# Kernel tuning notes

Hardware: AMD Instinct MI355X
Metric: run time of the kernel (lower is better)

## Reference

```python
import jax, jax.numpy as jnp
import numpy as np

N_EMBED = 1024
EMBED_DIM = 64
BETA = 0.25


def setup_inputs() -> dict:
    key = jax.random.key(0)
    k1, k2 = jax.random.split(key)
    x = jax.random.normal(k1, (32, EMBED_DIM, 64, 64), dtype=jnp.float32)  # NCHW, C == embed_dim
    embed = jax.random.uniform(
        k2, (N_EMBED, EMBED_DIM), dtype=jnp.float32,
        minval=-1.0 / N_EMBED, maxval=1.0 / N_EMBED,
    )
    return {"x": x, "embed": embed}


def reference(x, embed):
    # NCHW -> NHWC, flatten spatial+batch to rows of embed_dim
    z = jnp.transpose(x, (0, 2, 3, 1))                      # [B,H,W,D]
    zf = z.reshape(-1, EMBED_DIM)                           # [N,D]
    # squared L2 distance to every codeword: ||z||^2 + ||e||^2 - 2 z.e
    dist = (
        jnp.sum(zf * zf, axis=1, keepdims=True)
        + jnp.sum(embed * embed, axis=1)
        - 2.0 * zf @ embed.T
    )                                                       # [N, n_embed]
    idx = jnp.argmin(dist, axis=1)                          # [N]
    # one-hot @ embed == direct gather (same math, no scatter/matmul)
    z_q = embed[idx].reshape(z.shape)                       # [B,H,W,D]
    sg = jax.lax.stop_gradient
    loss = jnp.mean((sg(z_q) - z) ** 2) + BETA * jnp.mean((z_q - sg(z)) ** 2)
    # straight-through estimator
    z_q = z + sg(z_q - z)
    z_q = jnp.transpose(z_q, (0, 3, 1, 2))                  # back to NCHW
    return (z_q, loss)
```

## Files before the change

### kernel.cpp

```cpp
#include <hip/hip_runtime.h>


#define TOTAL_ELEMS 8388608
#define LOSS_SCALE (1.25f / 8388608.f)
#define ROWB 72

typedef float f32x4 __attribute__((ext_vector_type(4)));

static __device__ __forceinline__ void gload_lds16(const void* g, void* l) {
    __builtin_amdgcn_global_load_lds(
        (const __attribute__((address_space(1))) void*)g,
        (__attribute__((address_space(3))) void*)l,
        16, 0, 0);
}

static __device__ __forceinline__ unsigned int umax(unsigned int a, unsigned int b) {
    return a > b ? a : b;
}

__global__ void vq_prep(const float* __restrict__ embed,
                        unsigned char* __restrict__ eb,
                        float* __restrict__ c0,
                        float* __restrict__ loss_slot) {
    int t   = blockIdx.x * 256 + threadIdx.x;
    int row = t >> 2, qd = t & 3;
    const float* s0 = embed + row * 64 + qd * 8;
    const float* s1 = embed + row * 64 + 32 + qd * 8;
    f32x4 v0 = *(const f32x4*)s0, v1 = *(const f32x4*)(s0 + 4);
    f32x4 w0 = *(const f32x4*)s1, w1 = *(const f32x4*)(s1 + 4);
    float s = v0[0]*v0[0] + v0[1]*v0[1] + v0[2]*v0[2] + v0[3]*v0[3]
            + v1[0]*v1[0] + v1[1]*v1[1] + v1[2]*v1[2] + v1[3]*v1[3]
            + w0[0]*w0[0] + w0[1]*w0[1] + w0[2]*w0[2] + w0[3]*w0[3]
            + w1[0]*w1[0] + w1[1]*w1[1] + w1[2]*w1[2] + w1[3]*w1[3];
    unsigned int d0 = 0, d1 = 0, d2 = 0, d3 = 0;
    d0 = __builtin_amdgcn_cvt_pk_fp8_f32(v0[0]*1024.f, v0[1]*1024.f, d0, false);
    d0 = __builtin_amdgcn_cvt_pk_fp8_f32(v0[2]*1024.f, v0[3]*1024.f, d0, true);
    d1 = __builtin_amdgcn_cvt_pk_fp8_f32(v1[0]*1024.f, v1[1]*1024.f, d1, false);
    d1 = __builtin_amdgcn_cvt_pk_fp8_f32(v1[2]*1024.f, v1[3]*1024.f, d1, true);
    d2 = __builtin_amdgcn_cvt_pk_fp8_f32(w0[0]*1024.f, w0[1]*1024.f, d2, false);
    d2 = __builtin_amdgcn_cvt_pk_fp8_f32(w0[2]*1024.f, w0[3]*1024.f, d2, true);
    d3 = __builtin_amdgcn_cvt_pk_fp8_f32(w1[0]*1024.f, w1[1]*1024.f, d3, false);
    d3 = __builtin_amdgcn_cvt_pk_fp8_f32(w1[2]*1024.f, w1[3]*1024.f, d3, true);
    unsigned long long g0 = (unsigned long long)d0 | ((unsigned long long)d1 << 32);
    unsigned long long g1 = (unsigned long long)d2 | ((unsigned long long)d3 << 32);
    char* rb = (char*)eb + row * ROWB;
    *(unsigned long long*)(rb + qd * 8)      = g0;
    *(unsigned long long*)(rb + 32 + qd * 8) = g1;
    s += __shfl_xor(s, 1);
    s += __shfl_xor(s, 2);
    if (qd == 0) c0[row] = 64.f - 512.f * s;
    if (t == 0) *loss_slot = 0.f;
}

__global__ __launch_bounds__(512, 4) void vq_main(
    const float* __restrict__ x,
    const float* __restrict__ embed,
    const unsigned char* __restrict__ eb,
    const float* __restrict__ c0,
    float* __restrict__ out,
    float* __restrict__ loss) {

    __shared__ __align__(16) unsigned char cb[1024 * ROWB];
    __shared__ __align__(16) float c0l[1024];
    __shared__ float lpart[8];

    const int t    = threadIdx.x;
    const int wv   = t >> 6, lane = t & 63;
    const int l15  = lane & 15, lq = lane >> 4;

    const int blk = blockIdx.x;
    const int b   = blk >> 4;
    const int h0  = (blk & 15) * 4;
    const size_t xbase = (size_t)b * 262144 + (size_t)h0 * 64;
    const int rowoff = (wv >> 1) * 64 + (wv & 1) * 32;

    const char* ebp = (const char*)eb;

#pragma unroll
    for (int s = 0; s < 9; s++)
        gload_lds16(ebp + s * 8192 + t * 16, &cb[s * 8192 + t * 16]);

    if (t < 256) *(f32x4*)(c0l + t * 4) = *(const f32x4*)(c0 + t * 4);

    float part = 0.f;
    long bfr[2][2];
#pragma unroll
    for (int nt = 0; nt < 2; nt++) {
#pragma unroll
        for (int kh = 0; kh < 2; kh++) {
            unsigned int dw[2];
#pragma unroll
            for (int p = 0; p < 2; p++) {
                float f[4];
#pragma unroll
                for (int j = 0; j < 4; j++) {
                    f[j] = x[xbase + (size_t)(kh * 32 + lq * 8 + p * 4 + j) * 4096
                             + (size_t)rowoff + nt * 16 + l15];
                    part += f[j] * f[j];
                }
                unsigned int r = 0;
                r = __builtin_amdgcn_cvt_pk_fp8_f32(f[0], f[1], r, false);
                r = __builtin_amdgcn_cvt_pk_fp8_f32(f[2], f[3], r, true);
                dw[p] = r;
            }
            bfr[nt][kh] = (long)(((unsigned long long)dw[1] << 32) | dw[0]);
        }
    }
    __syncthreads();

    unsigned int key[2] = {0u, 0u};
    const unsigned char* bbase = &cb[l15 * ROWB + lq * 8];
    const float* cbase = c0l + lq * 4;
#pragma unroll 8
    for (int mt = 0; mt < 64; mt++) {
        long a0 = *(const long*)(bbase + mt * 16 * ROWB);
        long a1 = *(const long*)(bbase + mt * 16 * ROWB + 32);
        f32x4 c0v = *(const f32x4*)(cbase + mt * 16);
        const int invm = 1023 - mt * 16 - lq * 4;
#pragma unroll
        for (int nt = 0; nt < 2; nt++) {
            f32x4 acc = __builtin_amdgcn_mfma_f32_16x16x32_fp8_fp8(
                a0, bfr[nt][0], c0v, 0, 0, 0);
            acc = __builtin_amdgcn_mfma_f32_16x16x32_fp8_fp8(
                a1, bfr[nt][1], acc, 0, 0, 0);
            unsigned int k0 = (__float_as_uint(acc[0]) & 0xFFFFFC00u) | (unsigned int)(invm);
            unsigned int k1 = (__float_as_uint(acc[1]) & 0xFFFFFC00u) | (unsigned int)(invm - 1);
            unsigned int k2 = (__float_as_uint(acc[2]) & 0xFFFFFC00u) | (unsigned int)(invm - 2);
            unsigned int k3 = (__float_as_uint(acc[3]) & 0xFFFFFC00u) | (unsigned int)(invm - 3);
            key[nt] = umax(key[nt], umax(umax(k0, k1), umax(k2, k3)));
        }
    }

#pragma unroll
    for (int nt = 0; nt < 2; nt++) {
        unsigned int k = key[nt];
        unsigned int o = (unsigned int)__shfl_xor((int)k, 16); k = umax(k, o);
        o = (unsigned int)__shfl_xor((int)k, 32);              k = umax(k, o);
        key[nt] = k;
        part -= (1.f / 2048.f) * __uint_as_float(k & 0xFFFFFC00u);
    }

    unsigned int ks = ((lane >> 4) & 1) ? key[1] : key[0];
    const int idx = 1023 - (int)(ks & 1023u);

#pragma unroll
    for (int off = 1; off < 64; off <<= 1) part += __shfl_xor(part, off);
    if (lane == 0) lpart[wv] = part;

    const int ch0 = (lane >> 5) * 32;
    const int pos = lane & 31;
    const float* erow = embed + idx * 64 + ch0;
    float* orow = out + xbase + (size_t)rowoff + pos + (size_t)ch0 * 4096;
#pragma unroll
    for (int c4 = 0; c4 < 8; c4++) {
        f32x4 ev = *(const f32x4*)(erow + c4 * 4);
#pragma unroll
        for (int j = 0; j < 4; j++)
            orow[(size_t)(c4 * 4 + j) * 4096] = ev[j];
    }

    __syncthreads();
    if (t == 0) {
        float s = lpart[0] + lpart[1] + lpart[2] + lpart[3]
                + lpart[4] + lpart[5] + lpart[6] + lpart[7];
        atomicAdd(loss, (s + 32.0f) * LOSS_SCALE);
    }
}

extern "C" void kernel_launch(void* const* d_in, const int* in_sizes, int n_in,
                              void* d_out, int out_size, void* d_ws, size_t ws_size,
                              hipStream_t stream) {
    const float* x     = (const float*)d_in[0];
    const float* embed = (const float*)d_in[1];
    unsigned char* eb  = (unsigned char*)d_ws;
    float* c0          = (float*)((char*)d_ws + 73728);
    float* out  = (float*)d_out;
    float* loss = out + TOTAL_ELEMS;

    vq_prep<<<16, 256, 0, stream>>>(embed, eb, c0, loss);
    vq_main<<<512, 512, 0, stream>>>(x, embed, eb, c0, out, loss);
}
```

Measured before the change: 35.43 us.

## Split codebook sweep across four blocks with atomicMax key merge and separate output kernel

```diff
diff --git a/kernel.cpp b/kernel.cpp
--- a/kernel.cpp
+++ b/kernel.cpp
@@ -52,40 +52,40 @@
     if (t == 0) *loss_slot = 0.f;
 }
 
-__global__ __launch_bounds__(512, 4) void vq_main(
+__global__ __launch_bounds__(256, 8) void vq_sweep(
     const float* __restrict__ x,
-    const float* __restrict__ embed,
     const unsigned char* __restrict__ eb,
     const float* __restrict__ c0,
-    float* __restrict__ out,
+    unsigned int* __restrict__ keys,
     float* __restrict__ loss) {
 
-    __shared__ __align__(16) unsigned char cb[1024 * ROWB];
-    __shared__ __align__(16) float c0l[1024];
-    __shared__ float lpart[8];
+    __shared__ __align__(16) unsigned char cb[256 * ROWB];
+    __shared__ __align__(16) float c0l[256];
 
     const int t    = threadIdx.x;
     const int wv   = t >> 6, lane = t & 63;
     const int l15  = lane & 15, lq = lane >> 4;
 
-    const int blk = blockIdx.x;
-    const int b   = blk >> 4;
-    const int h0  = (blk & 15) * 4;
+    const int blk  = blockIdx.x;
+    const int q    = blk & 3;
+    const int tile = blk >> 2;
+    const int b    = tile >> 4;
+    const int h0   = (tile & 15) * 4;
     const size_t xbase = (size_t)b * 262144 + (size_t)h0 * 64;
-    const int rowoff = (wv >> 1) * 64 + (wv & 1) * 32;
-
-    const char* ebp = (const char*)eb;
-
-#pragma unroll
-    for (int s = 0; s < 9; s++)
-        gload_lds16(ebp + s * 8192 + t * 16, &cb[s * 8192 + t * 16]);
-
-    if (t < 256) *(f32x4*)(c0l + t * 4) = *(const f32x4*)(c0 + t * 4);
+
+    const char* ebq = (const char*)eb + q * (256 * ROWB);
+#pragma unroll
+    for (int s = 0; s < 4; s++)
+        gload_lds16(ebq + s * 4096 + t * 16, &cb[s * 4096 + t * 16]);
+    if (t < 128)
+        gload_lds16(ebq + 16384 + t * 16, &cb[16384 + t * 16]);
+
+    if (t < 64) *(f32x4*)(c0l + t * 4) = *(const f32x4*)(c0 + q * 256 + t * 4);
 
     float part = 0.f;
-    long bfr[2][2];
-#pragma unroll
-    for (int nt = 0; nt < 2; nt++) {
+    long bfr[4][2];
+#pragma unroll
+    for (int nt = 0; nt < 4; nt++) {
 #pragma unroll
         for (int kh = 0; kh < 2; kh++) {
             unsigned int dw[2];
@@ -95,7 +95,7 @@
 #pragma unroll
                 for (int j = 0; j < 4; j++) {
                     f[j] = x[xbase + (size_t)(kh * 32 + lq * 8 + p * 4 + j) * 4096
-                             + (size_t)rowoff + nt * 16 + l15];
+                             + (size_t)wv * 64 + nt * 16 + l15];
                     part += f[j] * f[j];
                 }
                 unsigned int r = 0;
@@ -108,17 +108,18 @@
     }
     __syncthreads();
 
-    unsigned int key[2] = {0u, 0u};
+    unsigned int key[4] = {0u, 0u, 0u, 0u};
     const unsigned char* bbase = &cb[l15 * ROWB + lq * 8];
     const float* cbase = c0l + lq * 4;
+    const int invq = 1023 - q * 256 - lq * 4;
 #pragma unroll 8
-    for (int mt = 0; mt < 64; mt++) {
+    for (int mt = 0; mt < 16; mt++) {
         long a0 = *(const long*)(bbase + mt * 16 * ROWB);
         long a1 = *(const long*)(bbase + mt * 16 * ROWB + 32);
         f32x4 c0v = *(const f32x4*)(cbase + mt * 16);
-        const int invm = 1023 - mt * 16 - lq * 4;
-#pragma unroll
-        for (int nt = 0; nt < 2; nt++) {
+        const int invm = invq - mt * 16;
+#pragma unroll
+        for (int nt = 0; nt < 4; nt++) {
             f32x4 acc = __builtin_amdgcn_mfma_f32_16x16x32_fp8_fp8(
                 a0, bfr[nt][0], c0v, 0, 0, 0);
             acc = __builtin_amdgcn_mfma_f32_16x16x32_fp8_fp8(
@@ -132,38 +133,58 @@
     }
 
 #pragma unroll
-    for (int nt = 0; nt < 2; nt++) {
+    for (int nt = 0; nt < 4; nt++) {
         unsigned int k = key[nt];
-        unsigned int o = (unsigned int)__shfl_xor((int)k, 16); k = umax(k, o);
-        o = (unsigned int)__shfl_xor((int)k, 32);              k = umax(k, o);
+        k = umax(k, (unsigned int)__shfl_xor((int)k, 16));
+        k = umax(k, (unsigned int)__shfl_xor((int)k, 32));
         key[nt] = k;
-        part -= (1.f / 2048.f) * __uint_as_float(k & 0xFFFFFC00u);
-    }
-
-    unsigned int ks = ((lane >> 4) & 1) ? key[1] : key[0];
-    const int idx = 1023 - (int)(ks & 1023u);
-
-#pragma unroll
-    for (int off = 1; off < 64; off <<= 1) part += __shfl_xor(part, off);
-    if (lane == 0) lpart[wv] = part;
-
-    const int ch0 = (lane >> 5) * 32;
-    const int pos = lane & 31;
-    const float* erow = embed + idx * 64 + ch0;
-    float* orow = out + xbase + (size_t)rowoff + pos + (size_t)ch0 * 4096;
+    }
+
+    unsigned int klo = (lane & 16) ? key[1] : key[0];
+    unsigned int khi = (lane & 16) ? key[3] : key[2];
+    unsigned int ks  = (lane & 32) ? khi : klo;
+    atomicMax(&keys[tile * 256 + wv * 64 + lane], ks);
+
+    if (q == 0) {
+#pragma unroll
+        for (int off = 1; off < 64; off <<= 1) part += __shfl_xor(part, off);
+        if (lane == 0) atomicAdd(loss, part * LOSS_SCALE);
+    }
+}
+
+__global__ void vq_out(
+    const unsigned int* __restrict__ keys,
+    const float* __restrict__ embed,
+    float* __restrict__ out,
+    float* __restrict__ loss) {
+
+    const int t    = threadIdx.x;
+    const int blk  = blockIdx.x;
+    const int tile = blk >> 1, ch = blk & 1;
+    const int b    = tile >> 4;
+    const int h0   = (tile & 15) * 4;
+    const int hh   = t >> 6, w = t & 63;
+
+    const unsigned int k = keys[tile * 256 + t];
+    const int idx = 1023 - (int)(k & 1023u);
+
+    if (ch == 0) {
+        float la = -(1.f / 512.f) * __uint_as_float(k & 0xFFFFFC00u);
+#pragma unroll
+        for (int off = 1; off < 64; off <<= 1) la += __shfl_xor(la, off);
+        if ((t & 63) == 0) atomicAdd(loss, (la + 8.0f) * LOSS_SCALE);
+    }
+
+    const int c0ch = ch * 32;
+    const float* erow = embed + idx * 64 + c0ch;
+    float* orow = out + (size_t)b * 262144 + (size_t)(h0 + hh) * 64 + w
+                + (size_t)c0ch * 4096;
 #pragma unroll
     for (int c4 = 0; c4 < 8; c4++) {
         f32x4 ev = *(const f32x4*)(erow + c4 * 4);
 #pragma unroll
         for (int j = 0; j < 4; j++)
             orow[(size_t)(c4 * 4 + j) * 4096] = ev[j];
-    }
-
-    __syncthreads();
-    if (t == 0) {
-        float s = lpart[0] + lpart[1] + lpart[2] + lpart[3]
-                + lpart[4] + lpart[5] + lpart[6] + lpart[7];
-        atomicAdd(loss, (s + 32.0f) * LOSS_SCALE);
     }
 }
 
@@ -172,11 +193,14 @@
                               hipStream_t stream) {
     const float* x     = (const float*)d_in[0];
     const float* embed = (const float*)d_in[1];
-    unsigned char* eb  = (unsigned char*)d_ws;
-    float* c0          = (float*)((char*)d_ws + 73728);
+    unsigned int* keys = (unsigned int*)d_ws;
+    unsigned char* eb  = (unsigned char*)d_ws + 524288;
+    float* c0          = (float*)((char*)d_ws + 524288 + 73728);
     float* out  = (float*)d_out;
     float* loss = out + TOTAL_ELEMS;
 
+    hipMemsetAsync(keys, 0, 131072 * sizeof(unsigned int), stream);
     vq_prep<<<16, 256, 0, stream>>>(embed, eb, c0, loss);
-    vq_main<<<512, 512, 0, stream>>>(x, embed, eb, c0, out, loss);
-}
+    vq_sweep<<<2048, 256, 0, stream>>>(x, eb, c0, keys, loss);
+    vq_out<<<1024, 256, 0, stream>>>(keys, embed, out, loss);
+}
```

After: 130.8 us. +269.1%, slower.
